# Kernel tuning notes

Hardware: AMD Instinct MI355X
Metric: run time of the kernel (lower is better)

The kernel has to match this reference:

```python
import jax, jax.numpy as jnp
import numpy as np
import math

B, S, D, H = 1, 2048, 2048, 16
DH, DHID, DKER = 128, 256, 128  # dim_head, dim_hid, dim_ker


def _uniform(k, shape, a):
    return jax.random.uniform(k, shape, jnp.float32, -a, a)


def setup_inputs() -> dict:
    key = jax.random.key(0)
    ks = jax.random.split(key, 14)
    a1 = math.sqrt(6.0 / (DH + DHID))
    a2 = math.sqrt(6.0 / (DKER + DHID))
    a3 = math.sqrt(6.0 / (2 * DKER))
    return {
        "x_t": jax.random.normal(ks[0], (B, S, D), jnp.float32),
        "q": jax.random.normal(ks[1], (B, S, D), jnp.float32),
        "k": jax.random.normal(ks[2], (B, S, D), jnp.float32),
        "v": jax.random.normal(ks[3], (B, S, D), jnp.float32),
        "lr_attn_mask": jax.random.bernoulli(ks[4], 0.5, (B, H, S, S)),
        "sparse_norms_lse": jax.random.normal(ks[5], (B, H, S, 1), jnp.float32),
        "sparse_attn_weights": jax.random.normal(ks[6], (B, H, S, S), jnp.float32),
        "lambda_constant": 0,
        "kernel_q_mat1": _uniform(ks[7], (H, DH, DHID), a1),
        "kernel_k_mat1": _uniform(ks[8], (H, DH, DHID), a1),
        "kernel_q_mat2": _uniform(ks[9], (H, DHID, DKER), a2),
        "kernel_k_mat2": _uniform(ks[10], (H, DHID, DKER), a2),
        "interaction_k": _uniform(ks[11], (H, DKER, DKER), a3),
        "scalingD": jnp.full((1, H, 1, DKER), 1e-4, jnp.float32),
        "scalingD2": jnp.full((1, H, 1, DKER), 1e-4, jnp.float32),
    }


def _gelu(x):
    return jax.nn.gelu(x, approximate=False)  # matches torch F.gelu default


def reference(x_t, q, k, v, lr_attn_mask, sparse_norms_lse, sparse_attn_weights,
              lambda_constant, kernel_q_mat1, kernel_k_mat1, kernel_q_mat2,
              kernel_k_mat2, interaction_k, scalingD, scalingD2):
    Bq, Sq, Dq = q.shape
    dh = Dq // H
    # [B,S,D] -> [B,H,S,dh]
    qh = q.reshape(Bq, Sq, H, dh).transpose(0, 2, 1, 3)
    kh = k.reshape(Bq, Sq, H, dh).transpose(0, 2, 1, 3)
    vh = v.reshape(Bq, Sq, H, dh).transpose(0, 2, 1, 3)

    # per-head two-layer feature maps (dropout is identity at eval)
    qf = _gelu(jnp.einsum('bhsd,hde->bhse', qh, kernel_q_mat1))
    qf = _gelu(jnp.einsum('bhse,hef->bhsf', qf, kernel_q_mat2))
    kf = _gelu(jnp.einsum('bhsd,hde->bhse', kh, kernel_k_mat1))
    kf = jnp.abs(scalingD) * _gelu(jnp.einsum('bhse,hef->bhsf', kf, kernel_k_mat2))
    kf = kf + jnp.einsum('bhse,hef->bhsf', kf, interaction_k) * scalingD2

    # masked non-negative kernel scores [B,H,S,S]
    scores = jnp.einsum('bhse,bhte->bhst', jnp.abs(qf), jnp.abs(kf))
    m = lr_attn_mask.astype(scores.dtype)
    scores = m * scores

    lr_norms_lse = jnp.log(scores.sum(axis=-1, keepdims=True) + 1e-6)
    norm_factor_lse = jnp.logaddexp(lr_norms_lse, sparse_norms_lse)

    logits = jnp.log(scores + 1e-6) * m + (1.0 - m) * sparse_attn_weights
    attn = jnp.exp(logits - norm_factor_lse)

    out = jnp.einsum('bhst,bhtd->bhsd', attn, vh)
    return out.transpose(0, 2, 1, 3).reshape(Bq, Sq, Dq)
```

## Files before the change

kernel.cpp:

```cpp
#include <hip/hip_runtime.h>
#include <hip/hip_bf16.h>
#include <math.h>

#define H_    16
#define S_    2048
#define D_    2048
#define DH_   128
#define DHID_ 256
#define DKER_ 128

typedef __attribute__((ext_vector_type(8))) short short8v;
typedef __attribute__((ext_vector_type(4))) float float4v;
typedef __attribute__((ext_vector_type(4))) int int4v;

static __device__ __forceinline__ short f2bf(float x){
  union { float f; unsigned u; } v; v.f = x;
  unsigned r = v.u + 0x7fffu + ((v.u >> 16) & 1u);
  return (short)(r >> 16);
}
static __device__ __forceinline__ float gelu_f(float x){
  return 0.5f * x * (1.0f + erff(x * 0.70710678118654752440f));
}
static __device__ __forceinline__ float4v mfma16(short8v a, short8v b, float4v c){
  return __builtin_amdgcn_mfma_f32_16x16x32_bf16(a, b, c, 0, 0, 0);
}
static __device__ __forceinline__ unsigned cvtpk(float lo, float hi){
  unsigned d;
  asm("v_cvt_pk_bf16_f32 %0, %1, %2" : "=v"(d) : "v"(lo), "v"(hi));
  return d;
}
static __device__ __forceinline__ void glds16(const void* g, void* l){
  __builtin_amdgcn_global_load_lds(
      (const __attribute__((address_space(1))) void*)g,
      (__attribute__((address_space(3))) void*)l, 16, 0, 0);
}

__global__ void detect_mask_kernel(const unsigned int* mw, int* flag){
  int t = threadIdx.x;
  int bin = 1, f32ok = 1, odd0 = 1;
  for (int i = t; i < 1024; i += 256){
    unsigned w = mw[i];
    if (w > 1u) bin = 0;
    if (w != 0u && w != 0x3F800000u) f32ok = 0;
    if ((i & 1) && w != 0u) odd0 = 0;
  }
  __shared__ int sb, sf, so;
  if (t == 0){ sb = 1; sf = 1; so = 1; }
  __syncthreads();
  if (!bin)  atomicAnd(&sb, 0);
  if (!f32ok) atomicAnd(&sf, 0);
  if (!odd0) atomicAnd(&so, 0);
  __syncthreads();
  if (t == 0) *flag = sb ? (so ? 3 : 0) : (sf ? 2 : 1);
}

__global__ __launch_bounds__(256) void prep_kernel(
    const void* __restrict__ mask, const int* __restrict__ flagp,
    unsigned* __restrict__ MP,
    const float* __restrict__ w1q, short* __restrict__ W1qT,
    const float* __restrict__ w1k, short* __restrict__ W1kT,
    const float* __restrict__ w2q, short* __restrict__ W2qT,
    const float* __restrict__ w2k, short* __restrict__ W2kT,
    const float* __restrict__ ik,  short* __restrict__ IKT,
    const float* __restrict__ v,   short* __restrict__ V2){
  __shared__ float tile[32][33];
  int b = blockIdx.x;
  int tid = threadIdx.x;

  if (b < 8192){
    int flag = *flagp;
    size_t w = (size_t)b * 256 + tid;
    size_t base = w * 32;
    unsigned bits = 0;
    if (flag == 0){
      const int4v* m = (const int4v*)((const int*)mask + base);
      #pragma unroll
      for (int c = 0; c < 8; ++c){
        int4v x = m[c];
        bits |= (x[0] != 0 ? 1u : 0u) << (c*4+0);
        bits |= (x[1] != 0 ? 1u : 0u) << (c*4+1);
        bits |= (x[2] != 0 ? 1u : 0u) << (c*4+2);
        bits |= (x[3] != 0 ? 1u : 0u) << (c*4+3);
      }
    } else if (flag == 1){
      const int4v* m = (const int4v*)((const unsigned char*)mask + base);
      #pragma unroll
      for (int c = 0; c < 2; ++c){
        int4v x = m[c];
        #pragma unroll
        for (int e = 0; e < 4; ++e){
          unsigned u = (unsigned)x[e];
          #pragma unroll
          for (int bb = 0; bb < 4; ++bb)
            bits |= (((u >> (8*bb)) & 0xffu) != 0 ? 1u : 0u) << (c*16 + e*4 + bb);
        }
      }
    } else if (flag == 2){
      const float4v* m = (const float4v*)((const float*)mask + base);
      #pragma unroll
      for (int c = 0; c < 8; ++c){
        float4v x = m[c];
        bits |= (x[0] != 0.0f ? 1u : 0u) << (c*4+0);
        bits |= (x[1] != 0.0f ? 1u : 0u) << (c*4+1);
        bits |= (x[2] != 0.0f ? 1u : 0u) << (c*4+2);
        bits |= (x[3] != 0.0f ? 1u : 0u) << (c*4+3);
      }
    } else {
      const int4v* m = (const int4v*)((const int*)mask + 2*base);
      #pragma unroll
      for (int c = 0; c < 16; ++c){
        int4v x = m[c];
        bits |= (x[0] != 0 ? 1u : 0u) << (c*2+0);
        bits |= (x[2] != 0 ? 1u : 0u) << (c*2+1);
      }
    }
    MP[w] = bits;
    return;
  }
  b -= 8192;
  if (b < 2048){
    int h = b >> 7, bx = b & 127;
    int d = tid & 127, oct = tid >> 7;
    int t8 = bx * 2 + oct;
    int t32 = t8 >> 2, o = t8 & 3;
    const float* src = v + (size_t)(t32 * 32) * D_ + h * DH_ + d;
    short8v ov;
    #pragma unroll
    for (int j = 0; j < 8; ++j){
      int trel = o * 4 + (j & 3) + ((j >> 2) << 4);
      ov[j] = f2bf(src[(size_t)trel * D_]);
    }
    *(short8v*)(V2 + (((size_t)h * (S_/8) + t8) * DH_ + d) * 8) = ov;
    return;
  }
  b -= 2048;
  const float* src; short* dst; int R, C, bx, by, h;
  if (b < 512){        src = w1q; dst = W1qT; R = DH_;  C = DHID_;
                       bx = b & 7; by = (b >> 3) & 3; h = b >> 5; }
  else if (b < 1024){  b -= 512;  src = w1k; dst = W1kT; R = DH_;  C = DHID_;
                       bx = b & 7; by = (b >> 3) & 3; h = b >> 5; }
  else if (b < 1536){  b -= 1024; src = w2q; dst = W2qT; R = DHID_; C = DKER_;
                       bx = b & 3; by = (b >> 2) & 7; h = b >> 5; }
  else if (b < 2048){  b -= 1536; src = w2k; dst = W2kT; R = DHID_; C = DKER_;
                       bx = b & 3; by = (b >> 2) & 7; h = b >> 5; }
  else {               b -= 2048; src = ik;  dst = IKT;  R = DKER_; C = DKER_;
                       bx = b & 3; by = (b >> 2) & 3; h = b >> 4; }
  int tx = tid & 31, ty = tid >> 5;
  int c0 = bx * 32, r0 = by * 32;
  const float* s = src + (size_t)h * R * C;
  short* d = dst + (size_t)h * R * C;
  #pragma unroll
  for (int i = 0; i < 32; i += 8)
    tile[ty + i][tx] = s[(size_t)(r0 + ty + i) * C + (c0 + tx)];
  __syncthreads();
  #pragma unroll
  for (int i = 0; i < 32; i += 8)
    d[(size_t)(c0 + ty + i) * R + (r0 + tx)] = f2bf(tile[tx][ty + i]);
}

__global__ __launch_bounds__(256) void feat_kernel(
    const float* __restrict__ q, const float* __restrict__ k,
    const short* __restrict__ W1qT, const short* __restrict__ W2qT,
    const short* __restrict__ W1kT, const short* __restrict__ W2kT,
    const short* __restrict__ IKT, const float* __restrict__ sD,
    const float* __restrict__ sD2,
    short* __restrict__ QF, short* __restrict__ KF){
  __shared__ __align__(16) short yls[4][16][264];
  int z = blockIdx.y;
  bool isq = z < 16;
  int h = z & 15;
  const float* X = isq ? q : k;
  const short* W1T = isq ? W1qT : W1kT;
  const short* W2T = isq ? W2qT : W2kT;
  int lane = threadIdx.x & 63, warp = threadIdx.x >> 6;
  int s0 = (blockIdx.x * 4 + warp) * 16;
  int col = lane & 15, rg = lane >> 4;
  short8v a[4];
  {
    const float* xr = X + (size_t)(s0 + col) * D_ + h * DH_;
    #pragma unroll
    for (int kb = 0; kb < 4; ++kb){
      int k0 = kb * 32 + rg * 8;
      float4v x0 = *(const float4v*)(xr + k0);
      float4v x1 = *(const float4v*)(xr + k0 + 4);
      short8v t;
      t[0]=f2bf(x0[0]); t[1]=f2bf(x0[1]); t[2]=f2bf(x0[2]); t[3]=f2bf(x0[3]);
      t[4]=f2bf(x1[0]); t[5]=f2bf(x1[1]); t[6]=f2bf(x1[2]); t[7]=f2bf(x1[3]);
      a[kb] = t;
    }
  }
  const short* wbase = W1T + (size_t)h * DHID_ * DH_;
  #pragma unroll
  for (int j = 0; j < 16; ++j){
    int n = j * 16;
    float4v c = {0.f, 0.f, 0.f, 0.f};
    const short* wr = wbase + (size_t)(n + col) * DH_ + rg * 8;
    #pragma unroll
    for (int kb = 0; kb < 4; ++kb)
      c = mfma16(a[kb], *(const short8v*)(wr + kb * 32), c);
    #pragma unroll
    for (int r = 0; r < 4; ++r)
      yls[warp][rg * 4 + r][n + col] = f2bf(gelu_f(c[r]));
  }
  short8v a2[8];
  #pragma unroll
  for (int kb = 0; kb < 8; ++kb)
    a2[kb] = *(const short8v*)(&yls[warp][col][kb * 32 + rg * 8]);
  const short* wb2 = W2T + (size_t)h * DKER_ * DHID_;

  if (isq){
    short* qb = QF + ((size_t)h * S_ + s0) * DKER_;
    #pragma unroll
    for (int j = 0; j < 8; ++j){
      int n = j * 16;
      float4v c = {0.f, 0.f, 0.f, 0.f};
      const short* wr = wb2 + (size_t)(n + col) * DHID_ + rg * 8;
      #pragma unroll
      for (int kb = 0; kb < 8; ++kb)
        c = mfma16(a2[kb], *(const short8v*)(wr + kb * 32), c);
      #pragma unroll
      for (int r = 0; r < 4; ++r)
        qb[(size_t)(rg * 4 + r) * DKER_ + n + col] = f2bf(fabsf(gelu_f(c[r])));
    }
    return;
  }
  float kf0[8][4];
  #pragma unroll
  for (int j = 0; j < 8; ++j){
    int n = j * 16;
    float4v c = {0.f, 0.f, 0.f, 0.f};
    const short* wr = wb2 + (size_t)(n + col) * DHID_ + rg * 8;
    #pragma unroll
    for (int kb = 0; kb < 8; ++kb)
      c = mfma16(a2[kb], *(const short8v*)(wr + kb * 32), c);
    float sc = fabsf(sD[h * DKER_ + n + col]);
    #pragma unroll
    for (int r = 0; r < 4; ++r) kf0[j][r] = sc * gelu_f(c[r]);
  }
  #pragma unroll
  for (int j = 0; j < 8; ++j)
    #pragma unroll
    for (int r = 0; r < 4; ++r)
      yls[warp][rg * 4 + r][j * 16 + col] = f2bf(kf0[j][r]);
  short8v pa[4];
  #pragma unroll
  for (int kb = 0; kb < 4; ++kb)
    pa[kb] = *(const short8v*)(&yls[warp][col][kb * 32 + rg * 8]);
  const short* ib = IKT + (size_t)h * DKER_ * DKER_;
  short* ko = KF + ((size_t)h * S_ + s0) * DKER_;
  #pragma unroll
  for (int j = 0; j < 8; ++j){
    int n = j * 16;
    float4v c = {0.f, 0.f, 0.f, 0.f};
    const short* ir = ib + (size_t)(n + col) * DKER_ + rg * 8;
    #pragma unroll
    for (int kb = 0; kb < 4; ++kb)
      c = mfma16(pa[kb], *(const short8v*)(ir + kb * 32), c);
    float s2 = sD2[h * DKER_ + n + col];
    #pragma unroll
    for (int r = 0; r < 4; ++r)
      ko[(size_t)(rg * 4 + r) * DKER_ + n + col] = f2bf(fabsf(kf0[j][r] + c[r] * s2));
  }
}

__global__ __launch_bounds__(512, 4) void main_attn_kernel(
    const short* __restrict__ QF, const short* __restrict__ KF,
    const short* __restrict__ V2, const unsigned* __restrict__ MP,
    const float* __restrict__ SW, const float* __restrict__ LSE,
    float* __restrict__ OUT){
  __shared__ __align__(16) char smem[65536];
  int tid = threadIdx.x;
  int lane = tid & 63, warp = tid >> 6;
  int hf = warp >> 2, w4 = warp & 3;
  int flat = blockIdx.y * 32 + blockIdx.x;
  int nf = (flat & 7) * 64 + (flat >> 3);
  int sblk = nf & 31, h = nf >> 5;
  int tbase = hf * (S_ / 2);
  int s0 = (sblk * 4 + w4) * 16;
  int col = lane & 15, rg = lane >> 4;

  short* kbuf = (short*)(smem + hf * 32768);
  short* vbuf = (short*)(smem + hf * 32768 + 16384);

  short8v qa[4];
  const short* qr = QF + ((size_t)h * S_ + s0 + col) * DKER_ + rg * 8;
  #pragma unroll
  for (int kb = 0; kb < 4; ++kb) qa[kb] = *(const short8v*)(qr + kb * 32);

  float4v acc[8];
  #pragma unroll
  for (int j = 0; j < 8; ++j) acc[j] = (float4v){0.f, 0.f, 0.f, 0.f};
  float rs = 0.f;

  const char* kf_base = (const char*)(KF + ((size_t)h * S_ + tbase) * DKER_);
  const char* v2_base = (const char*)(V2 + ((size_t)h * (S_/8) + (tbase >> 3)) * DH_ * 8);
  int c0 = w4 * 64 + lane, c1 = c0 + 256;
  int kg0 = (c0 * 16) ^ (((c0 >> 4) & 7) << 4);
  int kg1 = (c1 * 16) ^ (((c1 >> 4) & 7) << 4);
  int vg0 = c0 * 16, vg1 = c1 * 16;
  int lds_lo = w4 * 512, lds_hi = 2048 + w4 * 512;

  const float* swrow = SW + ((size_t)h * S_ + s0 + col) * S_ + tbase + rg * 4;
  const unsigned* mpr = MP + ((size_t)h * S_ + s0 + col) * (S_ / 32) + (tbase >> 5);

  {
    glds16(kf_base + kg0, &kbuf[lds_lo]);
    glds16(kf_base + kg1, &kbuf[lds_hi]);
    glds16(v2_base + vg0, &vbuf[lds_lo]);
    glds16(v2_base + vg1, &vbuf[lds_hi]);
  }
  __syncthreads();

  int swz = (col & 7) << 4;
  int rowb0 = col * 256 + rg * 16;
  const int NITER = (S_ / 2) / 32;

  for (int ti = 0; ti < NITER; ++ti){
    int cur = ti & 1;
    if (ti + 1 < NITER){
      const char* kt = kf_base + (size_t)(ti + 1) * 8192;
      const char* vt = v2_base + (size_t)(ti + 1) * 8192;
      glds16(kt + kg0, &kbuf[(cur ^ 1) * 4096 + lds_lo]);
      glds16(kt + kg1, &kbuf[(cur ^ 1) * 4096 + lds_hi]);
      glds16(vt + vg0, &vbuf[(cur ^ 1) * 4096 + lds_lo]);
      glds16(vt + vg1, &vbuf[(cur ^ 1) * 4096 + lds_hi]);
    }
    const char* kbp = (const char*)kbuf + cur * 8192;
    const char* vbp = (const char*)vbuf + cur * 8192;

    float4v q0 = {0.f,0.f,0.f,0.f}, q1 = {0.f,0.f,0.f,0.f};
    #pragma unroll
    for (int kk = 0; kk < 4; ++kk){
      short8v a0 = *(const short8v*)(kbp + ((rowb0 + kk * 64) ^ swz));
      short8v a1 = *(const short8v*)(kbp + ((rowb0 + 4096 + kk * 64) ^ swz));
      q0 = mfma16(a0, qa[kk], q0);
      q1 = mfma16(a1, qa[kk], q1);
    }

    const float* swp = swrow + ti * 32;
    float4v sv0 = *(const float4v*)swp;
    float4v sv1 = *(const float4v*)(swp + 16);
    unsigned mw = mpr[ti];
    float p0[4], p1[4];
    #pragma unroll
    for (int r = 0; r < 4; ++r){
      bool m0 = (mw >> (rg * 4 + r)) & 1u;
      bool m1 = (mw >> (16 + rg * 4 + r)) & 1u;
      p0[r] = m0 ? (q0[r] + 1e-6f) : __expf(sv0[r]);
      p1[r] = m1 ? (q1[r] + 1e-6f) : __expf(sv1[r]);
      if (m0) rs += q0[r];
      if (m1) rs += q1[r];
    }
    union { unsigned u[4]; short8v v8; } pw;
    pw.u[0] = cvtpk(p0[0], p0[1]); pw.u[1] = cvtpk(p0[2], p0[3]);
    pw.u[2] = cvtpk(p1[0], p1[1]); pw.u[3] = cvtpk(p1[2], p1[3]);
    short8v pa = pw.v8;

    #pragma unroll
    for (int j = 0; j < 8; ++j){
      short8v vf = *(const short8v*)(vbp + rg * 2048 + (j * 16 + col) * 16);
      acc[j] = mfma16(pa, vf, acc[j]);
    }
    __syncthreads();
  }

  rs += __shfl_xor(rs, 16);
  rs += __shfl_xor(rs, 32);

  __syncthreads();
  float* cb = (float*)smem;
  float* rb = (float*)(smem + 32768);
  if (hf == 1){
    float* cw = cb + (size_t)w4 * 16 * 128;
    #pragma unroll
    for (int j = 0; j < 8; ++j)
      #pragma unroll
      for (int r = 0; r < 4; ++r)
        cw[(size_t)(rg * 4 + r) * 128 + j * 16 + col] = acc[j][r];
    if (lane < 16) rb[w4 * 16 + lane] = rs;
  }
  __syncthreads();
  if (hf == 0){
    float* cw = cb + (size_t)w4 * 16 * 128;
    #pragma unroll
    for (int j = 0; j < 8; ++j)
      #pragma unroll
      for (int r = 0; r < 4; ++r)
        acc[j][r] += cw[(size_t)(rg * 4 + r) * 128 + j * 16 + col];
    rs += rb[w4 * 16 + col];

    float a = logf(rs + 1e-6f);
    float b = LSE[h * S_ + s0 + col];
    float mx = fmaxf(a, b);
    float sc_col = expf(-(mx + log1pf(expf(-fabsf(a - b)))));
    float scale[4];
    #pragma unroll
    for (int r = 0; r < 4; ++r) scale[r] = __shfl(sc_col, rg * 4 + r);
    float* ob = OUT + (size_t)s0 * D_ + h * DH_;
    #pragma unroll
    for (int j = 0; j < 8; ++j)
      #pragma unroll
      for (int r = 0; r < 4; ++r)
        ob[(size_t)(rg * 4 + r) * D_ + j * 16 + col] = acc[j][r] * scale[r];
  }
}

extern "C" void kernel_launch(void* const* d_in, const int* in_sizes, int n_in,
                              void* d_out, int out_size, void* d_ws, size_t ws_size,
                              hipStream_t stream){
  (void)in_sizes; (void)n_in; (void)out_size; (void)ws_size;
  const float* q   = (const float*)d_in[1];
  const float* k   = (const float*)d_in[2];
  const float* v   = (const float*)d_in[3];
  const void*  msk = d_in[4];
  const float* lse = (const float*)d_in[5];
  const float* sw  = (const float*)d_in[6];
  const float* w1q = (const float*)d_in[8];
  const float* w1k = (const float*)d_in[9];
  const float* w2q = (const float*)d_in[10];
  const float* w2k = (const float*)d_in[11];
  const float* ik  = (const float*)d_in[12];
  const float* sD  = (const float*)d_in[13];
  const float* sD2 = (const float*)d_in[14];
  float* out = (float*)d_out;

  char* ws = (char*)d_ws;
  size_t o = 0;
  int*   flag = (int*)(ws);            o += 256;
  short* W1qT = (short*)(ws + o);      o += (size_t)H_ * DHID_ * DH_ * 2;
  short* W1kT = (short*)(ws + o);      o += (size_t)H_ * DHID_ * DH_ * 2;
  short* W2qT = (short*)(ws + o);      o += (size_t)H_ * DKER_ * DHID_ * 2;
  short* W2kT = (short*)(ws + o);      o += (size_t)H_ * DKER_ * DHID_ * 2;
  short* IKT  = (short*)(ws + o);      o += (size_t)H_ * DKER_ * DKER_ * 2;
  short* V2   = (short*)(ws + o);      o += (size_t)S_ * D_ * 2;
  short* QFb  = (short*)(ws + o);      o += (size_t)H_ * S_ * DKER_ * 2;
  short* KFb  = (short*)(ws + o);      o += (size_t)H_ * S_ * DKER_ * 2;
  unsigned* MP = (unsigned*)(ws + o);  o += (size_t)H_ * S_ * (S_/32) * 4;

  detect_mask_kernel<<<1, 256, 0, stream>>>((const unsigned int*)msk, flag);
  prep_kernel<<<12544, 256, 0, stream>>>(msk, flag, MP,
      w1q, W1qT, w1k, W1kT, w2q, W2qT, w2k, W2kT, ik, IKT, v, V2);

  feat_kernel<<<dim3(S_/64, 32), 256, 0, stream>>>(q, k,
      W1qT, W2qT, W1kT, W2kT, IKT, sD, sD2, QFb, KFb);

  main_attn_kernel<<<dim3(32, 16), 512, 0, stream>>>(
      QFb, KFb, V2, MP, sw, lse, out);
}
```

Baseline: 248.4 us.

## Coalesce mask bit-packing, use tanh GELU, and packed bf16 conversion

Mask packing now has each thread read one contiguous 16-byte chunk (coalesced across the block) and produce a nibble, which is assembled into 32-bit words through shared memory. The grid grows accordingly. This replaces the old scheme where each thread read 128 strided bytes. GELU switches from erf to the tanh approximation via __expf, which cuts transcendental cost in the feature kernel but changes numerics slightly. Input bf16 conversion uses the packed v_cvt_pk_bf16_f32 instruction.

After: 235.2 us. 5.3% less time.

```diff
diff --git a/kernel.cpp b/kernel.cpp
--- a/kernel.cpp
+++ b/kernel.cpp
@@ -19,7 +19,10 @@
   return (short)(r >> 16);
 }
 static __device__ __forceinline__ float gelu_f(float x){
-  return 0.5f * x * (1.0f + erff(x * 0.70710678118654752440f));
+  float y = 0.7978845608028654f * (x + 0.044715f * x * x * x);
+  float e = __expf(2.0f * y);
+  float t = 1.0f - 2.0f / (e + 1.0f);
+  return 0.5f * x * (1.0f + t);
 }
 static __device__ __forceinline__ float4v mfma16(short8v a, short8v b, float4v c){
   return __builtin_amdgcn_mfma_f32_16x16x32_bf16(a, b, c, 0, 0, 0);
@@ -67,57 +70,37 @@
   int b = blockIdx.x;
   int tid = threadIdx.x;
 
-  if (b < 8192){
+  if (b < 65536){
+    __shared__ unsigned char nib[256];
     int flag = *flagp;
-    size_t w = (size_t)b * 256 + tid;
-    size_t base = w * 32;
-    unsigned bits = 0;
+    size_t g = (size_t)b * 256 + tid;
+    unsigned n = 0;
     if (flag == 0){
-      const int4v* m = (const int4v*)((const int*)mask + base);
-      #pragma unroll
-      for (int c = 0; c < 8; ++c){
-        int4v x = m[c];
-        bits |= (x[0] != 0 ? 1u : 0u) << (c*4+0);
-        bits |= (x[1] != 0 ? 1u : 0u) << (c*4+1);
-        bits |= (x[2] != 0 ? 1u : 0u) << (c*4+2);
-        bits |= (x[3] != 0 ? 1u : 0u) << (c*4+3);
-      }
+      int4v x = ((const int4v*)mask)[g];
+      n = (x[0]!=0 ? 1u:0u) | (x[1]!=0 ? 2u:0u) | (x[2]!=0 ? 4u:0u) | (x[3]!=0 ? 8u:0u);
     } else if (flag == 1){
-      const int4v* m = (const int4v*)((const unsigned char*)mask + base);
-      #pragma unroll
-      for (int c = 0; c < 2; ++c){
-        int4v x = m[c];
-        #pragma unroll
-        for (int e = 0; e < 4; ++e){
-          unsigned u = (unsigned)x[e];
-          #pragma unroll
-          for (int bb = 0; bb < 4; ++bb)
-            bits |= (((u >> (8*bb)) & 0xffu) != 0 ? 1u : 0u) << (c*16 + e*4 + bb);
-        }
-      }
+      unsigned x = ((const unsigned*)mask)[g];
+      n = ((x & 0xffu) ? 1u:0u) | ((x & 0xff00u) ? 2u:0u)
+        | ((x & 0xff0000u) ? 4u:0u) | ((x & 0xff000000u) ? 8u:0u);
     } else if (flag == 2){
-      const float4v* m = (const float4v*)((const float*)mask + base);
-      #pragma unroll
-      for (int c = 0; c < 8; ++c){
-        float4v x = m[c];
-        bits |= (x[0] != 0.0f ? 1u : 0u) << (c*4+0);
-        bits |= (x[1] != 0.0f ? 1u : 0u) << (c*4+1);
-        bits |= (x[2] != 0.0f ? 1u : 0u) << (c*4+2);
-        bits |= (x[3] != 0.0f ? 1u : 0u) << (c*4+3);
-      }
+      float4v x = ((const float4v*)mask)[g];
+      n = (x[0]!=0.f ? 1u:0u) | (x[1]!=0.f ? 2u:0u) | (x[2]!=0.f ? 4u:0u) | (x[3]!=0.f ? 8u:0u);
     } else {
-      const int4v* m = (const int4v*)((const int*)mask + 2*base);
-      #pragma unroll
-      for (int c = 0; c < 16; ++c){
-        int4v x = m[c];
-        bits |= (x[0] != 0 ? 1u : 0u) << (c*2+0);
-        bits |= (x[2] != 0 ? 1u : 0u) << (c*2+1);
-      }
-    }
-    MP[w] = bits;
+      int4v x0 = ((const int4v*)mask)[2*g];
+      int4v x1 = ((const int4v*)mask)[2*g+1];
+      n = (x0[0]!=0 ? 1u:0u) | (x0[2]!=0 ? 2u:0u) | (x1[0]!=0 ? 4u:0u) | (x1[2]!=0 ? 8u:0u);
+    }
+    nib[tid] = (unsigned char)n;
+    __syncthreads();
+    if (tid < 32){
+      unsigned w = 0;
+      #pragma unroll
+      for (int i = 0; i < 8; ++i) w |= (unsigned)nib[tid*8+i] << (4*i);
+      MP[(size_t)b * 32 + tid] = w;
+    }
     return;
   }
-  b -= 8192;
+  b -= 65536;
   if (b < 2048){
     int h = b >> 7, bx = b & 127;
     int d = tid & 127, oct = tid >> 7;
@@ -183,10 +166,10 @@
       int k0 = kb * 32 + rg * 8;
       float4v x0 = *(const float4v*)(xr + k0);
       float4v x1 = *(const float4v*)(xr + k0 + 4);
-      short8v t;
-      t[0]=f2bf(x0[0]); t[1]=f2bf(x0[1]); t[2]=f2bf(x0[2]); t[3]=f2bf(x0[3]);
-      t[4]=f2bf(x1[0]); t[5]=f2bf(x1[1]); t[6]=f2bf(x1[2]); t[7]=f2bf(x1[3]);
-      a[kb] = t;
+      union { unsigned u[4]; short8v v8; } t;
+      t.u[0] = cvtpk(x0[0], x0[1]); t.u[1] = cvtpk(x0[2], x0[3]);
+      t.u[2] = cvtpk(x1[0], x1[1]); t.u[3] = cvtpk(x1[2], x1[3]);
+      a[kb] = t.v8;
     }
   }
   const short* wbase = W1T + (size_t)h * DHID_ * DH_;
@@ -438,7 +421,7 @@
   unsigned* MP = (unsigned*)(ws + o);  o += (size_t)H_ * S_ * (S_/32) * 4;
 
   detect_mask_kernel<<<1, 256, 0, stream>>>((const unsigned int*)msk, flag);
-  prep_kernel<<<12544, 256, 0, stream>>>(msk, flag, MP,
+  prep_kernel<<<69888, 256, 0, stream>>>(msk, flag, MP,
       w1q, W1qT, w1k, W1kT, w2q, W2qT, w2k, W2kT, ik, IKT, v, V2);
 
   feat_kernel<<<dim3(S_/64, 32), 256, 0, stream>>>(q, k,
```
